# Performance work log

Measured on AMD Instinct MI355X. Metric: run time of the kernel, lower is better.

The kernel has to match this reference:

```python
import jax, jax.numpy as jnp
import numpy as np

B, T, D, H, L = 256, 128, 32, 512, 6
EPS = 1e-5


def setup_inputs() -> dict:
    key = jax.random.key(0)
    ks = jax.random.split(key, 12)
    sc = 0.02
    rn = lambda k, shp, s: (jax.random.normal(k, shp, jnp.float32) * s)
    return {
        "x": rn(ks[0], (B, T, D), 1.0),
        "w_proj": rn(ks[1], (H, D), sc),
        "b_proj": jnp.zeros((H,), jnp.float32),
        "w_ih": rn(ks[2], (L, 4 * H, H), sc),
        "w_hh": rn(ks[3], (L, 4 * H, H), sc),
        "b_ih": jnp.zeros((L, 4 * H), jnp.float32),
        "b_hh": jnp.zeros((L, 4 * H), jnp.float32),
        "ln_g": jnp.ones((L, H), jnp.float32),
        "ln_b": jnp.zeros((L, H), jnp.float32),
        "w1": rn(ks[4], (H, H), sc),
        "b1": jnp.zeros((H,), jnp.float32),
        "w2": rn(ks[5], (H // 2, H), sc),
        "b2": jnp.zeros((H // 2,), jnp.float32),
        "w3": rn(ks[6], (1, H // 2), sc),
        "b3": jnp.zeros((1,), jnp.float32),
    }


def _layer_norm(x, g, b):
    mu = jnp.mean(x, axis=-1, keepdims=True)
    var = jnp.mean(jnp.square(x - mu), axis=-1, keepdims=True)
    return (x - mu) * jax.lax.rsqrt(var + EPS) * g + b


def _lstm_layer(x, wih, whh, bih, bhh):
    # Precompute input-gate contributions for the whole sequence: [B,T,4H]
    xg = jnp.einsum("bth,gh->btg", x, wih) + (bih + bhh)
    h0 = jnp.zeros((x.shape[0], whh.shape[1]), x.dtype)

    def step(carry, xg_t):
        h, c = carry
        gates = xg_t + h @ whh.T  # [B,4H], torch gate order i,f,g,o
        i, f, g, o = jnp.split(gates, 4, axis=-1)
        i = jax.nn.sigmoid(i)
        f = jax.nn.sigmoid(f)
        g = jnp.tanh(g)
        o = jax.nn.sigmoid(o)
        c = f * c + i * g
        h = o * jnp.tanh(c)
        return (h, c), h

    _, hs = jax.lax.scan(step, (h0, h0), jnp.swapaxes(xg, 0, 1))  # hs: [T,B,H]
    return jnp.swapaxes(hs, 0, 1)  # [B,T,H]


def reference(x, w_proj, b_proj, w_ih, w_hh, b_ih, b_hh, ln_g, ln_b,
              w1, b1, w2, b2, w3, b3):
    h_prev = x @ w_proj.T + b_proj  # input projection: [B,T,H]
    for i in range(L):
        out = _lstm_layer(h_prev, w_ih[i], w_hh[i], b_ih[i], b_hh[i])
        out = _layer_norm(out, ln_g[i], ln_b[i])
        # dropout is identity in eval mode
        if i > 0:
            out = out + h_prev
        h_prev = out
    last = out[:, -1, :]  # [B,H]
    z = jax.nn.relu(last @ w1.T + b1)
    z = jax.nn.relu(z @ w2.T + b2)
    return z @ w3.T + b3  # [B,1]
```

## Files before the change

### kernel.cpp

```cpp
#include <hip/hip_runtime.h>
#include <hip/hip_bf16.h>
#include <stdint.h>

#define BB 256
#define TT 128
#define DD 32
#define HH 512
#define NL 6
#define TC 4

typedef __attribute__((ext_vector_type(8))) short short8;
typedef __attribute__((ext_vector_type(4))) float f32x4;

__device__ __forceinline__ unsigned short f2bf(float f) {
    union { float f; unsigned u; } v; v.f = f;
    unsigned r = v.u + 0x7fff + ((v.u >> 16) & 1);
    return (unsigned short)(r >> 16);
}
__device__ __forceinline__ float fsig(float x) { return 1.0f / (1.0f + __expf(-x)); }
__device__ __forceinline__ float ftanh(float x) {
    float e = __expf(-2.0f * fabsf(x));
    float t = (1.0f - e) / (1.0f + e);
    return x < 0.0f ? -t : t;
}

__global__ __launch_bounds__(256) void k_zero(unsigned int* __restrict__ p, int n) {
    int i = blockIdx.x * 256 + threadIdx.x;
    if (i < n) p[i] = 0;
}

__global__ __launch_bounds__(256) void k_convert(const float* __restrict__ wih, const float* __restrict__ whh,
                                                 unsigned short* __restrict__ wih_bf, unsigned short* __restrict__ whh_bf,
                                                 int n4) {
    int i = blockIdx.x * 256 + threadIdx.x;
    if (i >= n4) return;
    float4 a = ((const float4*)wih)[i];
    float4 b = ((const float4*)whh)[i];
    ushort4 ra; ra.x = f2bf(a.x); ra.y = f2bf(a.y); ra.z = f2bf(a.z); ra.w = f2bf(a.w);
    ushort4 rb; rb.x = f2bf(b.x); rb.y = f2bf(b.y); rb.z = f2bf(b.z); rb.w = f2bf(b.w);
    ((ushort4*)wih_bf)[i] = ra;
    ((ushort4*)whh_bf)[i] = rb;
}

__global__ __launch_bounds__(512) void k_proj(const float* __restrict__ x, const float* __restrict__ wp,
                                              const float* __restrict__ bp,
                                              float* __restrict__ hprev, unsigned short* __restrict__ abf) {
    __shared__ float xs[64][DD];
    int m0 = blockIdx.x * 64;
    for (int i = threadIdx.x; i < 64 * DD; i += 512)
        xs[i >> 5][i & 31] = x[(size_t)(m0 + (i >> 5)) * DD + (i & 31)];
    __syncthreads();
    int n = threadIdx.x;
    float w[DD];
#pragma unroll
    for (int k = 0; k < DD; k++) w[k] = wp[n * DD + k];
    float bias = bp[n];
    for (int r = 0; r < 64; r++) {
        float acc = bias;
#pragma unroll
        for (int k = 0; k < DD; k++) acc += xs[r][k] * w[k];
        size_t o = (size_t)(m0 + r) * HH + n;
        hprev[o] = acc;
        abf[o] = f2bf(acc);
    }
}

__global__ __launch_bounds__(256) void k_lstm_fused(const unsigned short* __restrict__ wih_bf,
                                                    const unsigned short* __restrict__ whh_bf,
                                                    const unsigned short* __restrict__ a_bf,
                                                    const float* __restrict__ bih, const float* __restrict__ bhh,
                                                    unsigned short* __restrict__ hbuf,
                                                    float* __restrict__ lstm_o,
                                                    unsigned int* __restrict__ cnt) {
    __shared__ unsigned short smem[64 * 512];
    const int blk = blockIdx.x;
    const int bx = (blk & 7) >> 1;
    const int ux = ((blk >> 3) << 1) | (blk & 1);
    const int tid = threadIdx.x, lane = tid & 63, w = tid >> 6;
    const int u0 = ux * 16;
    const int b0 = bx * 64 + w * 16;
    const int uu = lane & 15;
    const int kg = lane >> 4;
    unsigned int* cntp = cnt + bx * 64;

    for (int c = tid; c < 64 * 64; c += 256) {
        int rr = c >> 6, k16 = c & 63;
        int grow = ((rr >> 4) << 9) + u0 + (rr & 15);
        int4 v = *(const int4*)(whh_bf + (size_t)grow * 512 + k16 * 8);
        int baddr = (rr * 1024 + k16 * 16) ^ ((rr & 7) << 4);
        *(int4*)((char*)smem + baddr) = v;
    }
    __syncthreads();

    float biasg[4];
#pragma unroll
    for (int g = 0; g < 4; g++) biasg[g] = bih[(g << 9) + u0 + uu] + bhh[(g << 9) + u0 + uu];

    const int arow = b0 + uu;
    f32x4 cst = (f32x4){0.f, 0.f, 0.f, 0.f};
    f32x4 xacc[TC][4];

#pragma unroll 1
    for (int tc = 0; tc < TT; tc += TC) {
#pragma unroll
        for (int tt = 0; tt < TC; tt++)
#pragma unroll
            for (int g = 0; g < 4; g++)
                xacc[tt][g] = (f32x4){biasg[g], biasg[g], biasg[g], biasg[g]};
#pragma unroll
        for (int ks = 0; ks < 16; ks++) {
            short8 bfr[4];
#pragma unroll
            for (int g = 0; g < 4; g++)
                bfr[g] = *(const short8*)(wih_bf + (size_t)((g << 9) + u0 + uu) * 512 + ks * 32 + kg * 8);
#pragma unroll
            for (int tt = 0; tt < TC; tt++) {
                short8 afx = *(const short8*)(a_bf + ((size_t)arow * TT + (tc + tt)) * 512 + ks * 32 + kg * 8);
#pragma unroll
                for (int g = 0; g < 4; g++)
                    xacc[tt][g] = __builtin_amdgcn_mfma_f32_16x16x32_bf16(afx, bfr[g], xacc[tt][g], 0, 0, 0);
            }
        }
#pragma unroll
        for (int tt = 0; tt < TC; tt++) {
            const int t = tc + tt;
            if (t > 0) {
                if (tid == 0) {
                    unsigned target = 32u * (unsigned)t;
                    int guard = 0;
                    while (__hip_atomic_load(cntp, __ATOMIC_RELAXED, __HIP_MEMORY_SCOPE_AGENT) < target &&
                           ++guard < (1 << 18)) {}
                    (void)__hip_atomic_load(cntp, __ATOMIC_ACQUIRE, __HIP_MEMORY_SCOPE_AGENT);
                }
                __syncthreads();
                const unsigned short* hp = hbuf + (size_t)((t - 1) & 1) * (256 * 512);
                short8 ah[16];
#pragma unroll
                for (int ks = 0; ks < 16; ks++)
                    ah[ks] = *(const short8*)(hp + (size_t)arow * 512 + ks * 32 + kg * 8);
#pragma unroll
                for (int ks = 0; ks < 16; ks++) {
                    const int k2 = (ks * 32 + kg * 8) * 2;
#pragma unroll
                    for (int g = 0; g < 4; g++) {
                        const int rr = (g << 4) + uu;
                        const int baddr = (rr * 1024 + k2) ^ ((rr & 7) << 4);
                        short8 bh = *(const short8*)((const char*)smem + baddr);
                        xacc[tt][g] = __builtin_amdgcn_mfma_f32_16x16x32_bf16(ah[ks], bh, xacc[tt][g], 0, 0, 0);
                    }
                }
            }
            unsigned short* hw = hbuf + (size_t)(t & 1) * (256 * 512);
#pragma unroll
            for (int r = 0; r < 4; r++) {
                float i_ = fsig(xacc[tt][0][r]);
                float f_ = fsig(xacc[tt][1][r]);
                float g_ = ftanh(xacc[tt][2][r]);
                float o_ = fsig(xacc[tt][3][r]);
                float c = f_ * cst[r] + i_ * g_;
                cst[r] = c;
                float h = o_ * ftanh(c);
                int b = b0 + kg * 4 + r;
                lstm_o[((size_t)b * TT + t) * 512 + u0 + uu] = h;
                hw[(size_t)b * 512 + u0 + uu] = f2bf(h);
            }
            if (t < TT - 1) {
                __syncthreads();
                if (tid == 0)
                    __hip_atomic_fetch_add(cntp, 1u, __ATOMIC_RELEASE, __HIP_MEMORY_SCOPE_AGENT);
            }
        }
    }
}

__global__ __launch_bounds__(256) void k_ln(const float* __restrict__ xin, const float* __restrict__ resid,
                                            const float* __restrict__ g, const float* __restrict__ bta,
                                            float* __restrict__ hnew, unsigned short* __restrict__ abf,
                                            int do_res) {
    int row = blockIdx.x * 4 + (threadIdx.x >> 6);
    int lane = threadIdx.x & 63;
    const float* xr = xin + (size_t)row * 512;
    float vals[8];
    float s = 0.f, ss = 0.f;
#pragma unroll
    for (int i = 0; i < 2; i++) {
        float4 t = *(const float4*)(xr + lane * 8 + i * 4);
        vals[i * 4 + 0] = t.x; vals[i * 4 + 1] = t.y; vals[i * 4 + 2] = t.z; vals[i * 4 + 3] = t.w;
        s += t.x + t.y + t.z + t.w;
        ss += t.x * t.x + t.y * t.y + t.z * t.z + t.w * t.w;
    }
#pragma unroll
    for (int off = 32; off > 0; off >>= 1) {
        s += __shfl_down(s, off);
        ss += __shfl_down(ss, off);
    }
    s = __shfl(s, 0); ss = __shfl(ss, 0);
    float mu = s * (1.f / 512.f);
    float var = ss * (1.f / 512.f) - mu * mu;
    float rs = rsqrtf(var + 1e-5f);
#pragma unroll
    for (int i = 0; i < 8; i++) {
        int u = lane * 8 + i;
        float y = (vals[i] - mu) * rs * g[u] + bta[u];
        if (do_res) y += resid[(size_t)row * 512 + u];
        hnew[(size_t)row * 512 + u] = y;
        abf[(size_t)row * 512 + u] = f2bf(y);
    }
}

__global__ __launch_bounds__(512) void k_mlp1(const float* __restrict__ hprev, const float* __restrict__ w1,
                                              const float* __restrict__ b1, float* __restrict__ z1) {
    __shared__ float xs[512];
    int b = blockIdx.x;
    const float* xr = hprev + ((size_t)b * TT + (TT - 1)) * 512;
    xs[threadIdx.x] = xr[threadIdx.x];
    __syncthreads();
    int n = threadIdx.x;
    const float4* wr = (const float4*)(w1 + (size_t)n * 512);
    float acc = b1[n];
#pragma unroll 4
    for (int k4 = 0; k4 < 128; k4++) {
        float4 wv = wr[k4];
        acc += xs[k4 * 4 + 0] * wv.x + xs[k4 * 4 + 1] * wv.y + xs[k4 * 4 + 2] * wv.z + xs[k4 * 4 + 3] * wv.w;
    }
    z1[(size_t)b * 512 + n] = fmaxf(acc, 0.f);
}

__global__ __launch_bounds__(256) void k_mlp2(const float* __restrict__ z1, const float* __restrict__ w2,
                                              const float* __restrict__ b2, float* __restrict__ z2) {
    __shared__ float xs[512];
    int b = blockIdx.x;
    xs[threadIdx.x] = z1[(size_t)b * 512 + threadIdx.x];
    xs[threadIdx.x + 256] = z1[(size_t)b * 512 + threadIdx.x + 256];
    __syncthreads();
    int n = threadIdx.x;
    const float4* wr = (const float4*)(w2 + (size_t)n * 512);
    float acc = b2[n];
#pragma unroll 4
    for (int k4 = 0; k4 < 128; k4++) {
        float4 wv = wr[k4];
        acc += xs[k4 * 4 + 0] * wv.x + xs[k4 * 4 + 1] * wv.y + xs[k4 * 4 + 2] * wv.z + xs[k4 * 4 + 3] * wv.w;
    }
    z2[(size_t)b * 256 + n] = fmaxf(acc, 0.f);
}

__global__ __launch_bounds__(256) void k_mlp3(const float* __restrict__ z2, const float* __restrict__ w3,
                                              const float* __restrict__ b3, float* __restrict__ outp) {
    __shared__ float red[4];
    int b = blockIdx.x;
    int tid = threadIdx.x;
    float p = z2[(size_t)b * 256 + tid] * w3[tid];
#pragma unroll
    for (int off = 32; off > 0; off >>= 1) p += __shfl_down(p, off);
    if ((tid & 63) == 0) red[tid >> 6] = p;
    __syncthreads();
    if (tid == 0) outp[b] = red[0] + red[1] + red[2] + red[3] + b3[0];
}

extern "C" void kernel_launch(void* const* d_in, const int* in_sizes, int n_in,
                              void* d_out, int out_size, void* d_ws, size_t ws_size,
                              hipStream_t stream) {
    const float* x      = (const float*)d_in[0];
    const float* w_proj = (const float*)d_in[1];
    const float* b_proj = (const float*)d_in[2];
    const float* w_ih   = (const float*)d_in[3];
    const float* w_hh   = (const float*)d_in[4];
    const float* b_ih   = (const float*)d_in[5];
    const float* b_hh   = (const float*)d_in[6];
    const float* ln_g   = (const float*)d_in[7];
    const float* ln_b   = (const float*)d_in[8];
    const float* w1 = (const float*)d_in[9];  const float* b1 = (const float*)d_in[10];
    const float* w2 = (const float*)d_in[11]; const float* b2 = (const float*)d_in[12];
    const float* w3 = (const float*)d_in[13]; const float* b3 = (const float*)d_in[14];
    float* outp = (float*)d_out;

    char* ws = (char*)d_ws;
    size_t off = 0;
    auto alloc = [&](size_t sz) { char* p = ws + off; off += (sz + 255) & ~(size_t)255; return p; };
    unsigned short* a_bf   = (unsigned short*)alloc((size_t)32768 * 512 * 2);
    float*          lstm_o = (float*)alloc((size_t)32768 * 512 * 4);
    float*          hprev  = (float*)alloc((size_t)32768 * 512 * 4);
    unsigned short* wih_bf = (unsigned short*)alloc((size_t)NL * 2048 * 512 * 2);
    unsigned short* whh_bf = (unsigned short*)alloc((size_t)NL * 2048 * 512 * 2);
    unsigned short* hbuf   = (unsigned short*)alloc((size_t)2 * 256 * 512 * 2);
    float*          z1     = (float*)alloc((size_t)256 * 512 * 4);
    float*          z2     = (float*)alloc((size_t)256 * 256 * 4);
    unsigned int*   cnt    = (unsigned int*)alloc(2048 * 4);

    k_zero<<<8, 256, 0, stream>>>(cnt, 2048);
    k_convert<<<6144, 256, 0, stream>>>(w_ih, w_hh, wih_bf, whh_bf, (NL * 2048 * 512) / 4);
    k_proj<<<512, 512, 0, stream>>>(x, w_proj, b_proj, hprev, a_bf);

    for (int l = 0; l < NL; l++) {
        k_lstm_fused<<<128, 256, 0, stream>>>(wih_bf + (size_t)l * 2048 * 512,
                                              whh_bf + (size_t)l * 2048 * 512,
                                              a_bf, b_ih + l * 2048, b_hh + l * 2048,
                                              hbuf, lstm_o, cnt + l * 256);
        k_ln<<<8192, 256, 0, stream>>>(lstm_o, hprev, ln_g + l * 512, ln_b + l * 512,
                                       hprev, a_bf, l > 0 ? 1 : 0);
    }
    k_mlp1<<<256, 512, 0, stream>>>(hprev, w1, b1, z1);
    k_mlp2<<<256, 256, 0, stream>>>(z1, w2, b2, z2);
    k_mlp3<<<256, 256, 0, stream>>>(z2, w3, b3, outp);
}
```

Before: 9.281 ms.

## Interleave input-projection bursts with recurrent steps and use cache-bypassing h exchange

Moves the input-gate projection into two-step bursts that are interleaved between recurrent steps, so the W_ih work can fill the gap while waiting on the cross-block barrier. The hidden state exchange now uses inline asm loads and stores with sc0 sc1 bits that bypass caches, which replaces the acquire/release atomics with relaxed ones plus explicit waitcnt. h values are staged through shared memory so each thread writes a coalesced 8-byte chunk. The lstm_o store moves after the counter increment, taking it off the critical path. Memory ordering now depends on the cache-bypass bits rather than acquire semantics, which is subtle and risks correctness if those bits do not guarantee visibility.

```diff
diff --git a/kernel.cpp b/kernel.cpp
--- a/kernel.cpp
+++ b/kernel.cpp
@@ -7,7 +7,6 @@
 #define DD 32
 #define HH 512
 #define NL 6
-#define TC 4
 
 typedef __attribute__((ext_vector_type(8))) short short8;
 typedef __attribute__((ext_vector_type(4))) float f32x4;
@@ -22,6 +21,15 @@
     float e = __expf(-2.0f * fabsf(x));
     float t = (1.0f - e) / (1.0f + e);
     return x < 0.0f ? -t : t;
+}
+
+__device__ __forceinline__ int4 g_load16_cc(const void* p) {
+    int4 r;
+    asm volatile("global_load_dwordx4 %0, %1, off sc0 sc1" : "=v"(r) : "v"(p) : "memory");
+    return r;
+}
+__device__ __forceinline__ void g_store8_cc(void* p, unsigned long long v) {
+    asm volatile("global_store_dwordx2 %0, %1, off sc0 sc1" :: "v"(p), "v"(v) : "memory");
 }
 
 __global__ __launch_bounds__(256) void k_zero(unsigned int* __restrict__ p, int n) {
@@ -65,6 +73,96 @@
     }
 }
 
+__device__ __forceinline__ void do_burst(f32x4 (&X)[2][4], int TB,
+                                         const unsigned short* __restrict__ wih_bf,
+                                         const unsigned short* __restrict__ a_bf,
+                                         int u0, int uu, int kg, int arow, const float* biasg) {
+#pragma unroll
+    for (int tt = 0; tt < 2; tt++)
+#pragma unroll
+        for (int g = 0; g < 4; g++) X[tt][g] = (f32x4){biasg[g], biasg[g], biasg[g], biasg[g]};
+#pragma unroll
+    for (int ks = 0; ks < 16; ks++) {
+        short8 bfr[4];
+#pragma unroll
+        for (int g = 0; g < 4; g++)
+            bfr[g] = *(const short8*)(wih_bf + (size_t)((g << 9) + u0 + uu) * 512 + ks * 32 + kg * 8);
+#pragma unroll
+        for (int tt = 0; tt < 2; tt++) {
+            short8 afx = *(const short8*)(a_bf + ((size_t)arow * TT + (TB + tt)) * 512 + ks * 32 + kg * 8);
+#pragma unroll
+            for (int g = 0; g < 4; g++)
+                X[tt][g] = __builtin_amdgcn_mfma_f32_16x16x32_bf16(afx, bfr[g], X[tt][g], 0, 0, 0);
+        }
+    }
+}
+
+__device__ __forceinline__ void do_step(int T, f32x4 (&XR)[4], f32x4& cst,
+                                        const unsigned short* smem, unsigned short* hstage,
+                                        unsigned short* __restrict__ hbuf, float* __restrict__ lstm_o,
+                                        unsigned int* cntp,
+                                        int tid, int w, int uu, int kg, int u0, int b0, int bx, int arow) {
+    if (T > 0) {
+        if (tid == 0) {
+            unsigned target = 32u * (unsigned)T;
+            int guard = 0;
+            while (__hip_atomic_load(cntp, __ATOMIC_RELAXED, __HIP_MEMORY_SCOPE_AGENT) < target &&
+                   ++guard < (1 << 18)) {}
+        }
+        __syncthreads();
+        asm volatile("" ::: "memory");
+        const unsigned short* hp = hbuf + (size_t)((T - 1) & 1) * (256 * 512);
+        int4 ahi[16];
+#pragma unroll
+        for (int ks = 0; ks < 16; ks++)
+            ahi[ks] = g_load16_cc(hp + (size_t)arow * 512 + ks * 32 + kg * 8);
+        asm volatile("s_waitcnt vmcnt(0)" ::: "memory");
+        __builtin_amdgcn_sched_barrier(0);
+#pragma unroll
+        for (int ks = 0; ks < 16; ks++) {
+            short8 ah = *(short8*)&ahi[ks];
+            const int k2 = (ks * 32 + kg * 8) * 2;
+#pragma unroll
+            for (int g = 0; g < 4; g++) {
+                const int rr = (g << 4) + uu;
+                const int baddr = (rr * 1024 + k2) ^ ((rr & 7) << 4);
+                short8 bh = *(const short8*)((const char*)smem + baddr);
+                XR[g] = __builtin_amdgcn_mfma_f32_16x16x32_bf16(ah, bh, XR[g], 0, 0, 0);
+            }
+        }
+    }
+    float hval[4];
+#pragma unroll
+    for (int r = 0; r < 4; r++) {
+        float i_ = fsig(XR[0][r]);
+        float f_ = fsig(XR[1][r]);
+        float g_ = ftanh(XR[2][r]);
+        float o_ = fsig(XR[3][r]);
+        float c = f_ * cst[r] + i_ * g_;
+        cst[r] = c;
+        hval[r] = o_ * ftanh(c);
+    }
+#pragma unroll
+    for (int r = 0; r < 4; r++)
+        hstage[(w * 16 + kg * 4 + r) * 20 + uu] = f2bf(hval[r]);
+    __syncthreads();
+    {
+        int bb = tid >> 2, uoff = (tid & 3) * 4;
+        unsigned long long hv = *(const unsigned long long*)(hstage + bb * 20 + uoff);
+        unsigned short* hw = hbuf + (size_t)(T & 1) * (256 * 512);
+        g_store8_cc(hw + (size_t)(bx * 64 + bb) * 512 + u0 + uoff, hv);
+    }
+    asm volatile("s_waitcnt vmcnt(0)" ::: "memory");
+    __syncthreads();
+    if (T < TT - 1 && tid == 0)
+        __hip_atomic_fetch_add(cntp, 1u, __ATOMIC_RELAXED, __HIP_MEMORY_SCOPE_AGENT);
+#pragma unroll
+    for (int r = 0; r < 4; r++) {
+        int b = b0 + kg * 4 + r;
+        lstm_o[((size_t)b * TT + T) * 512 + u0 + uu] = hval[r];
+    }
+}
+
 __global__ __launch_bounds__(256) void k_lstm_fused(const unsigned short* __restrict__ wih_bf,
                                                     const unsigned short* __restrict__ whh_bf,
                                                     const unsigned short* __restrict__ a_bf,
@@ -73,6 +171,7 @@
                                                     float* __restrict__ lstm_o,
                                                     unsigned int* __restrict__ cnt) {
     __shared__ unsigned short smem[64 * 512];
+    __shared__ unsigned short hstage[64 * 20];
     const int blk = blockIdx.x;
     const int bx = (blk & 7) >> 1;
     const int ux = ((blk >> 3) << 1) | (blk & 1);
@@ -98,78 +197,19 @@
 
     const int arow = b0 + uu;
     f32x4 cst = (f32x4){0.f, 0.f, 0.f, 0.f};
-    f32x4 xacc[TC][4];
+    f32x4 xA[2][4], xB[2][4];
+
+    do_burst(xA, 0, wih_bf, a_bf, u0, uu, kg, arow, biasg);
 
 #pragma unroll 1
-    for (int tc = 0; tc < TT; tc += TC) {
-#pragma unroll
-        for (int tt = 0; tt < TC; tt++)
-#pragma unroll
-            for (int g = 0; g < 4; g++)
-                xacc[tt][g] = (f32x4){biasg[g], biasg[g], biasg[g], biasg[g]};
-#pragma unroll
-        for (int ks = 0; ks < 16; ks++) {
-            short8 bfr[4];
-#pragma unroll
-            for (int g = 0; g < 4; g++)
-                bfr[g] = *(const short8*)(wih_bf + (size_t)((g << 9) + u0 + uu) * 512 + ks * 32 + kg * 8);
-#pragma unroll
-            for (int tt = 0; tt < TC; tt++) {
-                short8 afx = *(const short8*)(a_bf + ((size_t)arow * TT + (tc + tt)) * 512 + ks * 32 + kg * 8);
-#pragma unroll
-                for (int g = 0; g < 4; g++)
-                    xacc[tt][g] = __builtin_amdgcn_mfma_f32_16x16x32_bf16(afx, bfr[g], xacc[tt][g], 0, 0, 0);
-            }
-        }
-#pragma unroll
-        for (int tt = 0; tt < TC; tt++) {
-            const int t = tc + tt;
-            if (t > 0) {
-                if (tid == 0) {
-                    unsigned target = 32u * (unsigned)t;
-                    int guard = 0;
-                    while (__hip_atomic_load(cntp, __ATOMIC_RELAXED, __HIP_MEMORY_SCOPE_AGENT) < target &&
-                           ++guard < (1 << 18)) {}
-                    (void)__hip_atomic_load(cntp, __ATOMIC_ACQUIRE, __HIP_MEMORY_SCOPE_AGENT);
-                }
-                __syncthreads();
-                const unsigned short* hp = hbuf + (size_t)((t - 1) & 1) * (256 * 512);
-                short8 ah[16];
-#pragma unroll
-                for (int ks = 0; ks < 16; ks++)
-                    ah[ks] = *(const short8*)(hp + (size_t)arow * 512 + ks * 32 + kg * 8);
-#pragma unroll
-                for (int ks = 0; ks < 16; ks++) {
-                    const int k2 = (ks * 32 + kg * 8) * 2;
-#pragma unroll
-                    for (int g = 0; g < 4; g++) {
-                        const int rr = (g << 4) + uu;
-                        const int baddr = (rr * 1024 + k2) ^ ((rr & 7) << 4);
-                        short8 bh = *(const short8*)((const char*)smem + baddr);
-                        xacc[tt][g] = __builtin_amdgcn_mfma_f32_16x16x32_bf16(ah[ks], bh, xacc[tt][g], 0, 0, 0);
-                    }
-                }
-            }
-            unsigned short* hw = hbuf + (size_t)(t & 1) * (256 * 512);
-#pragma unroll
-            for (int r = 0; r < 4; r++) {
-                float i_ = fsig(xacc[tt][0][r]);
-                float f_ = fsig(xacc[tt][1][r]);
-                float g_ = ftanh(xacc[tt][2][r]);
-                float o_ = fsig(xacc[tt][3][r]);
-                float c = f_ * cst[r] + i_ * g_;
-                cst[r] = c;
-                float h = o_ * ftanh(c);
-                int b = b0 + kg * 4 + r;
-                lstm_o[((size_t)b * TT + t) * 512 + u0 + uu] = h;
-                hw[(size_t)b * 512 + u0 + uu] = f2bf(h);
-            }
-            if (t < TT - 1) {
-                __syncthreads();
-                if (tid == 0)
-                    __hip_atomic_fetch_add(cntp, 1u, __ATOMIC_RELEASE, __HIP_MEMORY_SCOPE_AGENT);
-            }
-        }
+    for (int tc = 0; tc < TT; tc += 4) {
+        do_step(tc + 0, xA[0], cst, smem, hstage, hbuf, lstm_o, cntp, tid, w, uu, kg, u0, b0, bx, arow);
+        do_burst(xB, tc + 2, wih_bf, a_bf, u0, uu, kg, arow, biasg);
+        do_step(tc + 1, xA[1], cst, smem, hstage, hbuf, lstm_o, cntp, tid, w, uu, kg, u0, b0, bx, arow);
+        do_step(tc + 2, xB[0], cst, smem, hstage, hbuf, lstm_o, cntp, tid, w, uu, kg, u0, b0, bx, arow);
+        if (tc + 4 < TT)
+            do_burst(xA, tc + 4, wih_bf, a_bf, u0, uu, kg, arow, biasg);
+        do_step(tc + 3, xB[1], cst, smem, hstage, hbuf, lstm_o, cntp, tid, w, uu, kg, u0, b0, bx, arow);
     }
 }
 
```

After: 8.774 ms. 1.06x faster.

## Fuse all LSTM layers and layernorm into one wavefront-pipelined persistent kernel

Applied to the files above, without the earlier changes.

Replaces the six per-layer LSTM launches and separate layernorm kernels with one persistent kernel of 192 blocks (32 per layer). Layers run concurrently in a wavefront over timesteps, synchronised through global counters, and layernorm plus the residual add is fused in. Activations pass between layers through a 16-slot bf16 ring buffer instead of full fp32 sequence tensors, which removes the large lstm_o/hprev traffic and the serial dependence between layers. In exchange it adds cross-block spin synchronisation with bounded guards, cache-bypassing loads and stores, bf16 rounding of the residual path, and a reliance on all 192 blocks being co-resident.

```diff
diff --git a/kernel.cpp b/kernel.cpp
--- a/kernel.cpp
+++ b/kernel.cpp
@@ -7,7 +7,6 @@
 #define DD 32
 #define HH 512
 #define NL 6
-#define TC 4
 
 typedef __attribute__((ext_vector_type(8))) short short8;
 typedef __attribute__((ext_vector_type(4))) float f32x4;
@@ -16,12 +15,34 @@
     union { float f; unsigned u; } v; v.f = f;
     unsigned r = v.u + 0x7fff + ((v.u >> 16) & 1);
     return (unsigned short)(r >> 16);
+}
+__device__ __forceinline__ float bf2f(unsigned short s) {
+    union { unsigned u; float f; } v; v.u = ((unsigned)s) << 16;
+    return v.f;
 }
 __device__ __forceinline__ float fsig(float x) { return 1.0f / (1.0f + __expf(-x)); }
 __device__ __forceinline__ float ftanh(float x) {
     float e = __expf(-2.0f * fabsf(x));
     float t = (1.0f - e) / (1.0f + e);
     return x < 0.0f ? -t : t;
+}
+
+__device__ __forceinline__ int4 g_load16_cc(const void* p) {
+    int4 r;
+    asm volatile("global_load_dwordx4 %0, %1, off sc0 sc1" : "=v"(r) : "v"(p) : "memory");
+    return r;
+}
+__device__ __forceinline__ void g_store16_cc(void* p, int4 v) {
+    union { int4 q; unsigned long long d[2]; } u; u.q = v;
+    void* p2 = (void*)((char*)p + 8);
+    asm volatile("global_store_dwordx2 %0, %1, off sc0 sc1" :: "v"(p), "v"(u.d[0]) : "memory");
+    asm volatile("global_store_dwordx2 %0, %1, off sc0 sc1" :: "v"(p2), "v"(u.d[1]) : "memory");
+}
+
+__device__ __forceinline__ void poll_ge(unsigned int* p, unsigned target) {
+    int guard = 0;
+    while (__hip_atomic_load(p, __ATOMIC_RELAXED, __HIP_MEMORY_SCOPE_AGENT) < target &&
+           ++guard < (1 << 17)) {}
 }
 
 __global__ __launch_bounds__(256) void k_zero(unsigned int* __restrict__ p, int n) {
@@ -44,7 +65,7 @@
 
 __global__ __launch_bounds__(512) void k_proj(const float* __restrict__ x, const float* __restrict__ wp,
                                               const float* __restrict__ bp,
-                                              float* __restrict__ hprev, unsigned short* __restrict__ abf) {
+                                              unsigned short* __restrict__ abf) {
     __shared__ float xs[64][DD];
     int m0 = blockIdx.x * 64;
     for (int i = threadIdx.x; i < 64 * DD; i += 512)
@@ -59,161 +80,271 @@
         float acc = bias;
 #pragma unroll
         for (int k = 0; k < DD; k++) acc += xs[r][k] * w[k];
-        size_t o = (size_t)(m0 + r) * HH + n;
-        hprev[o] = acc;
-        abf[o] = f2bf(acc);
-    }
-}
-
-__global__ __launch_bounds__(256) void k_lstm_fused(const unsigned short* __restrict__ wih_bf,
-                                                    const unsigned short* __restrict__ whh_bf,
-                                                    const unsigned short* __restrict__ a_bf,
-                                                    const float* __restrict__ bih, const float* __restrict__ bhh,
-                                                    unsigned short* __restrict__ hbuf,
-                                                    float* __restrict__ lstm_o,
-                                                    unsigned int* __restrict__ cnt) {
-    __shared__ unsigned short smem[64 * 512];
+        abf[(size_t)(m0 + r) * HH + n] = f2bf(acc);
+    }
+}
+
+__device__ __forceinline__ void do_ln(int l, int tln, int row, int li, bool final_out,
+                                      const unsigned short* __restrict__ hbuf,
+                                      unsigned short* __restrict__ xring,
+                                      const float* __restrict__ ln_g, const float* __restrict__ ln_b,
+                                      float* __restrict__ xfinal) {
+    const unsigned short* hrow = hbuf + ((size_t)(l * 2 + (tln & 1))) * 131072 + (size_t)row * 512 + li * 16;
+    int4 h0 = g_load16_cc(hrow);
+    int4 h1 = g_load16_cc(hrow + 8);
+    int4 r0, r1;
+    const bool res = (l > 0);
+    if (res) {
+        const unsigned short* xrow = xring + ((size_t)((l - 1) * 16 + (tln & 15))) * 131072 + (size_t)row * 512 + li * 16;
+        r0 = g_load16_cc(xrow);
+        r1 = g_load16_cc(xrow + 8);
+    }
+    asm volatile("s_waitcnt vmcnt(0)" ::: "memory");
+    __builtin_amdgcn_sched_barrier(0);
+    const unsigned short* hu0 = (const unsigned short*)&h0;
+    const unsigned short* hu1 = (const unsigned short*)&h1;
+    float v[16];
+    float s = 0.f, ss = 0.f;
+#pragma unroll
+    for (int e = 0; e < 8; e++) { v[e] = bf2f(hu0[e]); v[e + 8] = bf2f(hu1[e]); }
+#pragma unroll
+    for (int e = 0; e < 16; e++) { s += v[e]; ss += v[e] * v[e]; }
+#pragma unroll
+    for (int off = 1; off < 32; off <<= 1) {
+        s += __shfl_xor(s, off);
+        ss += __shfl_xor(ss, off);
+    }
+    float mu = s * (1.f / 512.f);
+    float var = ss * (1.f / 512.f) - mu * mu;
+    float rs = rsqrtf(var + 1e-5f);
+    const unsigned short* ru0 = (const unsigned short*)&r0;
+    const unsigned short* ru1 = (const unsigned short*)&r1;
+    float y[16];
+#pragma unroll
+    for (int e = 0; e < 16; e++) {
+        float yy = (v[e] - mu) * rs * ln_g[l * 512 + li * 16 + e] + ln_b[l * 512 + li * 16 + e];
+        if (res) yy += bf2f(e < 8 ? ru0[e] : ru1[e - 8]);
+        y[e] = yy;
+    }
+    if (final_out) {
+        float* dst = xfinal + (size_t)row * 512 + li * 16;
+#pragma unroll
+        for (int q = 0; q < 4; q++)
+            *(float4*)(dst + q * 4) = (float4){y[q * 4], y[q * 4 + 1], y[q * 4 + 2], y[q * 4 + 3]};
+    } else {
+        unsigned short ys[16];
+#pragma unroll
+        for (int e = 0; e < 16; e++) ys[e] = f2bf(y[e]);
+        unsigned short* dst = xring + ((size_t)(l * 16 + (tln & 15))) * 131072 + (size_t)row * 512 + li * 16;
+        g_store16_cc(dst, *(int4*)&ys[0]);
+        g_store16_cc(dst + 8, *(int4*)&ys[8]);
+    }
+}
+
+__global__ __launch_bounds__(256, 1) void k_mega(
+    const unsigned short* __restrict__ wih_bf,
+    const unsigned short* __restrict__ whh_bf,
+    const unsigned short* __restrict__ a_bf,
+    const float* __restrict__ bih_all, const float* __restrict__ bhh_all,
+    const float* __restrict__ ln_g, const float* __restrict__ ln_b,
+    unsigned short* __restrict__ xring,
+    unsigned short* __restrict__ hbuf,
+    float* __restrict__ xfinal,
+    unsigned int* __restrict__ cnt)
+{
+    __shared__ unsigned short smem[128 * 512];
+    __shared__ unsigned short hstage[128 * 40];
+
     const int blk = blockIdx.x;
-    const int bx = (blk & 7) >> 1;
-    const int ux = ((blk >> 3) << 1) | (blk & 1);
+    const int l = blk >> 5;
+    const int rr_ = blk & 31;
+    const int g = rr_ >> 4;
+    const int ui = rr_ & 15;
     const int tid = threadIdx.x, lane = tid & 63, w = tid >> 6;
-    const int u0 = ux * 16;
-    const int b0 = bx * 64 + w * 16;
+    const int u0 = ui * 32;
+    const int gb0 = g * 128;
+    const int wb0 = gb0 + w * 32;
     const int uu = lane & 15;
     const int kg = lane >> 4;
-    unsigned int* cntp = cnt + bx * 64;
-
-    for (int c = tid; c < 64 * 64; c += 256) {
+
+    const unsigned short* wih = wih_bf + (size_t)l * 2048 * 512;
+    const unsigned short* whh = whh_bf + (size_t)l * 2048 * 512;
+    unsigned int* c1  = cnt + (l * 2 + g) * 64;
+    unsigned int* c1n = cnt + ((l + 1) * 2 + g) * 64;
+    unsigned int* c2  = cnt + (12 + l * 2 + g) * 64;
+    unsigned int* c2u = cnt + (12 + (l - 1) * 2 + g) * 64;
+
+    for (int c = tid; c < 128 * 64; c += 256) {
         int rr = c >> 6, k16 = c & 63;
-        int grow = ((rr >> 4) << 9) + u0 + (rr & 15);
-        int4 v = *(const int4*)(whh_bf + (size_t)grow * 512 + k16 * 8);
+        int grow = (rr >> 5) * 512 + u0 + ((rr >> 4) & 1) * 16 + (rr & 15);
+        int4 v = *(const int4*)(whh + (size_t)grow * 512 + k16 * 8);
         int baddr = (rr * 1024 + k16 * 16) ^ ((rr & 7) << 4);
         *(int4*)((char*)smem + baddr) = v;
     }
     __syncthreads();
 
-    float biasg[4];
-#pragma unroll
-    for (int g = 0; g < 4; g++) biasg[g] = bih[(g << 9) + u0 + uu] + bhh[(g << 9) + u0 + uu];
-
-    const int arow = b0 + uu;
-    f32x4 cst = (f32x4){0.f, 0.f, 0.f, 0.f};
-    f32x4 xacc[TC][4];
+    float biasg[8];
+#pragma unroll
+    for (int rt = 0; rt < 8; rt++) {
+        int grow = (rt >> 1) * 512 + u0 + ((rt & 1) << 4) + uu;
+        biasg[rt] = bih_all[l * 2048 + grow] + bhh_all[l * 2048 + grow];
+    }
+
+    const int ln_row = gb0 + ui * 8 + w * 2 + (lane >> 5);
+    const int li = lane & 31;
+    f32x4 cst[4];
+#pragma unroll
+    for (int q = 0; q < 4; q++) cst[q] = (f32x4){0.f, 0.f, 0.f, 0.f};
 
 #pragma unroll 1
-    for (int tc = 0; tc < TT; tc += TC) {
-#pragma unroll
-        for (int tt = 0; tt < TC; tt++)
-#pragma unroll
-            for (int g = 0; g < 4; g++)
-                xacc[tt][g] = (f32x4){biasg[g], biasg[g], biasg[g], biasg[g]};
-#pragma unroll
-        for (int ks = 0; ks < 16; ks++) {
-            short8 bfr[4];
-#pragma unroll
-            for (int g = 0; g < 4; g++)
-                bfr[g] = *(const short8*)(wih_bf + (size_t)((g << 9) + u0 + uu) * 512 + ks * 32 + kg * 8);
-#pragma unroll
-            for (int tt = 0; tt < TC; tt++) {
-                short8 afx = *(const short8*)(a_bf + ((size_t)arow * TT + (tc + tt)) * 512 + ks * 32 + kg * 8);
-#pragma unroll
-                for (int g = 0; g < 4; g++)
-                    xacc[tt][g] = __builtin_amdgcn_mfma_f32_16x16x32_bf16(afx, bfr[g], xacc[tt][g], 0, 0, 0);
+    for (int t = 0; t < TT; ++t) {
+        if (tid == 0) {
+            if (t > 0) poll_ge(c1, 16u * (unsigned)t);
+            if (l < 5 && t >= 17) poll_ge(c1n, 16u * (unsigned)(t - 15));
+        }
+        __syncthreads();
+
+        if (t > 0 && l < 5) {
+            do_ln(l, t - 1, ln_row, li, false, hbuf, xring, ln_g, ln_b, xfinal);
+            asm volatile("s_waitcnt vmcnt(0)" ::: "memory");
+            __syncthreads();
+            if (tid == 0)
+                __hip_atomic_fetch_add(c2, 1u, __ATOMIC_RELAXED, __HIP_MEMORY_SCOPE_AGENT);
+        }
+
+        if (l > 0) {
+            if (tid == 0) poll_ge(c2u, 16u * (unsigned)(t + 1));
+            __syncthreads();
+        }
+
+        f32x4 acc[2][8];
+#pragma unroll
+        for (int bt = 0; bt < 2; bt++)
+#pragma unroll
+            for (int rt = 0; rt < 8; rt++)
+                acc[bt][rt] = (f32x4){biasg[rt], biasg[rt], biasg[rt], biasg[rt]};
+
+#pragma unroll
+        for (int half = 0; half < 2; half++) {
+            short8 ax[2][8];
+            if (l == 0) {
+#pragma unroll
+                for (int bt = 0; bt < 2; bt++)
+#pragma unroll
+                    for (int k8 = 0; k8 < 8; k8++)
+                        ax[bt][k8] = *(const short8*)(a_bf + ((size_t)(wb0 + bt * 16 + uu) * TT + t) * 512 +
+                                                      (half * 8 + k8) * 32 + kg * 8);
+            } else {
+                const unsigned short* xs = xring + ((size_t)((l - 1) * 16 + (t & 15))) * 131072;
+                int4 ai[2][8];
+#pragma unroll
+                for (int bt = 0; bt < 2; bt++)
+#pragma unroll
+                    for (int k8 = 0; k8 < 8; k8++)
+                        ai[bt][k8] = g_load16_cc(xs + (size_t)(wb0 + bt * 16 + uu) * 512 +
+                                                 (half * 8 + k8) * 32 + kg * 8);
+                asm volatile("s_waitcnt vmcnt(0)" ::: "memory");
+                __builtin_amdgcn_sched_barrier(0);
+#pragma unroll
+                for (int bt = 0; bt < 2; bt++)
+#pragma unroll
+                    for (int k8 = 0; k8 < 8; k8++)
+                        ax[bt][k8] = *(short8*)&ai[bt][k8];
             }
-        }
-#pragma unroll
-        for (int tt = 0; tt < TC; tt++) {
-            const int t = tc + tt;
-            if (t > 0) {
-                if (tid == 0) {
-                    unsigned target = 32u * (unsigned)t;
-                    int guard = 0;
-                    while (__hip_atomic_load(cntp, __ATOMIC_RELAXED, __HIP_MEMORY_SCOPE_AGENT) < target &&
-                           ++guard < (1 << 18)) {}
-                    (void)__hip_atomic_load(cntp, __ATOMIC_ACQUIRE, __HIP_MEMORY_SCOPE_AGENT);
+#pragma unroll
+            for (int k8 = 0; k8 < 8; k8++) {
+                int ks = half * 8 + k8;
+#pragma unroll
+                for (int rt = 0; rt < 8; rt++) {
+                    short8 bfr = *(const short8*)(wih + (size_t)((rt >> 1) * 512 + u0 + ((rt & 1) << 4) + uu) * 512 +
+                                                  ks * 32 + kg * 8);
+                    acc[0][rt] = __builtin_amdgcn_mfma_f32_16x16x32_bf16(ax[0][k8], bfr, acc[0][rt], 0, 0, 0);
+                    acc[1][rt] = __builtin_amdgcn_mfma_f32_16x16x32_bf16(ax[1][k8], bfr, acc[1][rt], 0, 0, 0);
                 }
-                __syncthreads();
-                const unsigned short* hp = hbuf + (size_t)((t - 1) & 1) * (256 * 512);
-                short8 ah[16];
-#pragma unroll
-                for (int ks = 0; ks < 16; ks++)
-                    ah[ks] = *(const short8*)(hp + (size_t)arow * 512 + ks * 32 + kg * 8);
-#pragma unroll
-                for (int ks = 0; ks < 16; ks++) {
-                    const int k2 = (ks * 32 + kg * 8) * 2;
-#pragma unroll
-                    for (int g = 0; g < 4; g++) {
-                        const int rr = (g << 4) + uu;
-                        const int baddr = (rr * 1024 + k2) ^ ((rr & 7) << 4);
+            }
+        }
+
+        if (t > 0) {
+            const unsigned short* hp = hbuf + ((size_t)(l * 2 + ((t - 1) & 1))) * 131072;
+#pragma unroll
+            for (int half = 0; half < 2; half++) {
+                int4 ai[2][8];
+#pragma unroll
+                for (int bt = 0; bt < 2; bt++)
+#pragma unroll
+                    for (int k8 = 0; k8 < 8; k8++)
+                        ai[bt][k8] = g_load16_cc(hp + (size_t)(wb0 + bt * 16 + uu) * 512 +
+                                                 (half * 8 + k8) * 32 + kg * 8);
+                asm volatile("s_waitcnt vmcnt(0)" ::: "memory");
+                __builtin_amdgcn_sched_barrier(0);
+#pragma unroll
+                for (int k8 = 0; k8 < 8; k8++) {
+                    int k2 = ((half * 8 + k8) * 32 + kg * 8) * 2;
+                    short8 ah0 = *(short8*)&ai[0][k8];
+                    short8 ah1 = *(short8*)&ai[1][k8];
+#pragma unroll
+                    for (int rt = 0; rt < 8; rt++) {
+                        int rr = rt * 16 + uu;
+                        int baddr = (rr * 1024 + k2) ^ ((rr & 7) << 4);
                         short8 bh = *(const short8*)((const char*)smem + baddr);
-                        xacc[tt][g] = __builtin_amdgcn_mfma_f32_16x16x32_bf16(ah[ks], bh, xacc[tt][g], 0, 0, 0);
+                        acc[0][rt] = __builtin_amdgcn_mfma_f32_16x16x32_bf16(ah0, bh, acc[0][rt], 0, 0, 0);
+                        acc[1][rt] = __builtin_amdgcn_mfma_f32_16x16x32_bf16(ah1, bh, acc[1][rt], 0, 0, 0);
                     }
                 }
             }
-            unsigned short* hw = hbuf + (size_t)(t & 1) * (256 * 512);
-#pragma unroll
-            for (int r = 0; r < 4; r++) {
-                float i_ = fsig(xacc[tt][0][r]);
-                float f_ = fsig(xacc[tt][1][r]);
-                float g_ = ftanh(xacc[tt][2][r]);
-                float o_ = fsig(xacc[tt][3][r]);
-                float c = f_ * cst[r] + i_ * g_;
-                cst[r] = c;
-                float h = o_ * ftanh(c);
-                int b = b0 + kg * 4 + r;
-                lstm_o[((size_t)b * TT + t) * 512 + u0 + uu] = h;
-                hw[(size_t)b * 512 + u0 + uu] = f2bf(h);
+        }
+
+#pragma unroll
+        for (int bt = 0; bt < 2; bt++)
+#pragma unroll
+            for (int usub = 0; usub < 2; usub++) {
+                f32x4 iq = acc[bt][0 + usub], fq = acc[bt][2 + usub];
+                f32x4 gq = acc[bt][4 + usub], oq = acc[bt][6 + usub];
+#pragma unroll
+                for (int j = 0; j < 4; j++) {
+                    float i_ = fsig(iq[j]);
+                    float f_ = fsig(fq[j]);
+                    float g_ = ftanh(gq[j]);
+                    float o_ = fsig(oq[j]);
+                    float c = f_ * cst[bt * 2 + usub][j] + i_ * g_;
+                    cst[bt * 2 + usub][j] = c;
+                    float h = o_ * ftanh(c);
+                    hstage[(w * 32 + bt * 16 + kg * 4 + j) * 40 + usub * 16 + uu] = f2bf(h);
+                }
             }
-            if (t < TT - 1) {
-                __syncthreads();
-                if (tid == 0)
-                    __hip_atomic_fetch_add(cntp, 1u, __ATOMIC_RELEASE, __HIP_MEMORY_SCOPE_AGENT);
-            }
-        }
-    }
-}
-
-__global__ __launch_bounds__(256) void k_ln(const float* __restrict__ xin, const float* __restrict__ resid,
-                                            const float* __restrict__ g, const float* __restrict__ bta,
-                                            float* __restrict__ hnew, unsigned short* __restrict__ abf,
-                                            int do_res) {
-    int row = blockIdx.x * 4 + (threadIdx.x >> 6);
-    int lane = threadIdx.x & 63;
-    const float* xr = xin + (size_t)row * 512;
-    float vals[8];
-    float s = 0.f, ss = 0.f;
-#pragma unroll
-    for (int i = 0; i < 2; i++) {
-        float4 t = *(const float4*)(xr + lane * 8 + i * 4);
-        vals[i * 4 + 0] = t.x; vals[i * 4 + 1] = t.y; vals[i * 4 + 2] = t.z; vals[i * 4 + 3] = t.w;
-        s += t.x + t.y + t.z + t.w;
-        ss += t.x * t.x + t.y * t.y + t.z * t.z + t.w * t.w;
-    }
-#pragma unroll
-    for (int off = 32; off > 0; off >>= 1) {
-        s += __shfl_down(s, off);
-        ss += __shfl_down(ss, off);
-    }
-    s = __shfl(s, 0); ss = __shfl(ss, 0);
-    float mu = s * (1.f / 512.f);
-    float var = ss * (1.f / 512.f) - mu * mu;
-    float rs = rsqrtf(var + 1e-5f);
-#pragma unroll
-    for (int i = 0; i < 8; i++) {
-        int u = lane * 8 + i;
-        float y = (vals[i] - mu) * rs * g[u] + bta[u];
-        if (do_res) y += resid[(size_t)row * 512 + u];
-        hnew[(size_t)row * 512 + u] = y;
-        abf[(size_t)row * 512 + u] = f2bf(y);
-    }
-}
-
-__global__ __launch_bounds__(512) void k_mlp1(const float* __restrict__ hprev, const float* __restrict__ w1,
+        __syncthreads();
+        {
+            int lb = tid >> 1, hf = tid & 1;
+            int4 v0 = *(const int4*)(hstage + lb * 40 + hf * 16);
+            int4 v1 = *(const int4*)(hstage + lb * 40 + hf * 16 + 8);
+            unsigned short* hd = hbuf + ((size_t)(l * 2 + (t & 1))) * 131072 + (size_t)(gb0 + lb) * 512 + u0 + hf * 16;
+            g_store16_cc(hd, v0);
+            g_store16_cc(hd + 8, v1);
+        }
+        asm volatile("s_waitcnt vmcnt(0)" ::: "memory");
+        __syncthreads();
+        if (tid == 0)
+            __hip_atomic_fetch_add(c1, 1u, __ATOMIC_RELAXED, __HIP_MEMORY_SCOPE_AGENT);
+    }
+
+    if (tid == 0) poll_ge(c1, 16u * 128u);
+    __syncthreads();
+    if (l < 5) {
+        do_ln(l, TT - 1, ln_row, li, false, hbuf, xring, ln_g, ln_b, xfinal);
+        asm volatile("s_waitcnt vmcnt(0)" ::: "memory");
+        __syncthreads();
+        if (tid == 0)
+            __hip_atomic_fetch_add(c2, 1u, __ATOMIC_RELAXED, __HIP_MEMORY_SCOPE_AGENT);
+    } else {
+        do_ln(l, TT - 1, ln_row, li, true, hbuf, xring, ln_g, ln_b, xfinal);
+    }
+}
+
+__global__ __launch_bounds__(512) void k_mlp1(const float* __restrict__ xfinal, const float* __restrict__ w1,
                                               const float* __restrict__ b1, float* __restrict__ z1) {
     __shared__ float xs[512];
     int b = blockIdx.x;
-    const float* xr = hprev + ((size_t)b * TT + (TT - 1)) * 512;
-    xs[threadIdx.x] = xr[threadIdx.x];
+    xs[threadIdx.x] = xfinal[(size_t)b * 512 + threadIdx.x];
     __syncthreads();
     int n = threadIdx.x;
     const float4* wr = (const float4*)(w1 + (size_t)n * 512);
@@ -278,28 +409,23 @@
     size_t off = 0;
     auto alloc = [&](size_t sz) { char* p = ws + off; off += (sz + 255) & ~(size_t)255; return p; };
     unsigned short* a_bf   = (unsigned short*)alloc((size_t)32768 * 512 * 2);
-    float*          lstm_o = (float*)alloc((size_t)32768 * 512 * 4);
-    float*          hprev  = (float*)alloc((size_t)32768 * 512 * 4);
     unsigned short* wih_bf = (unsigned short*)alloc((size_t)NL * 2048 * 512 * 2);
     unsigned short* whh_bf = (unsigned short*)alloc((size_t)NL * 2048 * 512 * 2);
-    unsigned short* hbuf   = (unsigned short*)alloc((size_t)2 * 256 * 512 * 2);
+    unsigned short* xring  = (unsigned short*)alloc((size_t)5 * 16 * 256 * 512 * 2);
+    unsigned short* hbuf   = (unsigned short*)alloc((size_t)6 * 2 * 256 * 512 * 2);
+    float*          xfinal = (float*)alloc((size_t)256 * 512 * 4);
     float*          z1     = (float*)alloc((size_t)256 * 512 * 4);
     float*          z2     = (float*)alloc((size_t)256 * 256 * 4);
     unsigned int*   cnt    = (unsigned int*)alloc(2048 * 4);
 
     k_zero<<<8, 256, 0, stream>>>(cnt, 2048);
     k_convert<<<6144, 256, 0, stream>>>(w_ih, w_hh, wih_bf, whh_bf, (NL * 2048 * 512) / 4);
-    k_proj<<<512, 512, 0, stream>>>(x, w_proj, b_proj, hprev, a_bf);
-
-    for (int l = 0; l < NL; l++) {
-        k_lstm_fused<<<128, 256, 0, stream>>>(wih_bf + (size_t)l * 2048 * 512,
-                                              whh_bf + (size_t)l * 2048 * 512,
-                                              a_bf, b_ih + l * 2048, b_hh + l * 2048,
-                                              hbuf, lstm_o, cnt + l * 256);
-        k_ln<<<8192, 256, 0, stream>>>(lstm_o, hprev, ln_g + l * 512, ln_b + l * 512,
-                                       hprev, a_bf, l > 0 ? 1 : 0);
-    }
-    k_mlp1<<<256, 512, 0, stream>>>(hprev, w1, b1, z1);
+    k_proj<<<512, 512, 0, stream>>>(x, w_proj, b_proj, a_bf);
+
+    k_mega<<<192, 256, 0, stream>>>(wih_bf, whh_bf, a_bf, b_ih, b_hh, ln_g, ln_b,
+                                    xring, hbuf, xfinal, cnt);
+
+    k_mlp1<<<256, 512, 0, stream>>>(xfinal, w1, b1, z1);
     k_mlp2<<<256, 256, 0, stream>>>(z1, w2, b2, z2);
     k_mlp3<<<256, 256, 0, stream>>>(z2, w3, b3, outp);
 }
```

Result: no change. 9.298 ms (+0.2%).
